# Performance work log

Hardware: AMD Instinct MI355X
Metric: run time of the kernel (lower is better)

## Reference

```python
import jax, jax.numpy as jnp
import numpy as np

N = 100000          # nodes
E = 800000          # edges
H = 32              # hidden_features
L = 4               # num_layers
HS = 32             # hidden_edge_scores
EPS_BN = 1e-5
EPS_AGG = 1e-6


def _bn(x, g, b):
    # training-mode batch norm over the node/edge (batch) axis
    mu = jnp.mean(x, axis=0)
    var = jnp.var(x, axis=0)
    return (x - mu) * jax.lax.rsqrt(var + EPS_BN) * g + b


def setup_inputs() -> dict:
    key = jax.random.key(0)
    ks = jax.random.split(key, 24)
    rn = lambda k, s, sc=0.1: jax.random.normal(k, s, dtype=jnp.float32) * sc
    return {
        "x": rn(ks[0], (N, 1), 1.0),
        "e": rn(ks[1], (E, 1), 1.0),
        "edge_index": jax.random.randint(ks[2], (2, E), 0, N),
        # input projections
        "pe_w": rn(ks[3], (1, H)), "pe_b": rn(ks[4], (H,)),
        "ed_w": rn(ks[5], (1, H)), "ed_b": rn(ks[6], (H,)),
        # per-layer GatedGCN weights, stacked over layers
        "A_w": rn(ks[7], (L, H, H)), "A_b": rn(ks[8], (L, H)),
        "B_w": rn(ks[9], (L, H, H)), "B_b": rn(ks[10], (L, H)),
        "C_w": rn(ks[11], (L, H, H)), "C_b": rn(ks[12], (L, H)),
        "U_w": rn(ks[13], (L, H, H)), "U_b": rn(ks[14], (L, H)),
        "V_w": rn(ks[15], (L, H, H)), "V_b": rn(ks[16], (L, H)),
        # batch-norm affine params
        "bn_h_g": jnp.ones((L, H), jnp.float32), "bn_h_b": jnp.zeros((L, H), jnp.float32),
        "bn_e_g": jnp.ones((L, H), jnp.float32), "bn_e_b": jnp.zeros((L, H), jnp.float32),
        # score predictor: concat(src_h, dst_h, e) -> HS -> 1
        "W1_w": rn(ks[17], (3 * H, HS)), "W1_b": rn(ks[18], (HS,)),
        "W2_w": rn(ks[19], (HS, 1)), "W2_b": rn(ks[20], (1,)),
    }


def reference(x, e, edge_index, pe_w, pe_b, ed_w, ed_b,
              A_w, A_b, B_w, B_b, C_w, C_b, U_w, U_b, V_w, V_b,
              bn_h_g, bn_h_b, bn_e_g, bn_e_b, W1_w, W1_b, W2_w, W2_b):
    src, dst = edge_index[0], edge_index[1]
    h = x @ pe_w + pe_b          # [N, H]
    e = e @ ed_w + ed_b          # [E, H]
    n = h.shape[0]
    for l in range(L):
        Ah = h @ A_w[l] + A_b[l]
        Bh = h @ B_w[l] + B_b[l]
        Ce = e @ C_w[l] + C_b[l]
        Uh = h @ U_w[l] + U_b[l]
        Vh = h @ V_w[l] + V_b[l]
        # edge update: gather node features to edges
        e_new = Ah[dst] + Bh[src] + Ce               # [E, H]
        sigma = jax.nn.sigmoid(e_new)                # edge gates
        # gated mean aggregation: scatter-add to dst nodes
        num = jax.ops.segment_sum(sigma * Vh[src], dst, num_segments=n)
        den = jax.ops.segment_sum(sigma, dst, num_segments=n)
        h_new = Uh + num / (den + EPS_AGG)           # [N, H]
        # BN -> ReLU -> residual
        h = h + jax.nn.relu(_bn(h_new, bn_h_g[l], bn_h_b[l]))
        e = e + jax.nn.relu(_bn(e_new, bn_e_g[l], bn_e_b[l]))
    # score predictor over edges
    z = jnp.concatenate([h[src], h[dst], e], axis=1)  # [E, 3H]
    scores = jax.nn.relu(z @ W1_w + W1_b) @ W2_w + W2_b  # [E, 1]
    return scores
```

## Files before the change

### kernel.cpp

```cpp
#include <hip/hip_runtime.h>
#include <hip/hip_bf16.h>
#include <hip/hip_fp16.h>

#define NLAYERS 4
#define GRID_STRIDE 2048

typedef _Float16 half8_t __attribute__((ext_vector_type(8)));
typedef float float4_t __attribute__((ext_vector_type(4)));
typedef float float8_t __attribute__((ext_vector_type(8)));

__global__ void zero_ints(int* __restrict__ p, int n)
{
    int i = blockIdx.x * 256 + threadIdx.x;
    if (i < n) p[i] = 0;
}

__global__ void hist_kernel(const int* __restrict__ dsts, int* __restrict__ counts, int E)
{
    int i = blockIdx.x * 256 + threadIdx.x;
    if (i < E) atomicAdd(&counts[dsts[i]], 1);
}

__global__ __launch_bounds__(256) void scan1(const int* __restrict__ counts,
                                             int* __restrict__ offsets,
                                             int* __restrict__ blocksums, int N)
{
    __shared__ int sdata[256];
    int t = threadIdx.x;
    int bbase = blockIdx.x * 1024;
    int v[4]; int s = 0;
#pragma unroll
    for (int q = 0; q < 4; q++) {
        int idx = bbase + t * 4 + q;
        v[q] = (idx < N) ? counts[idx] : 0;
        s += v[q];
    }
    sdata[t] = s;
    __syncthreads();
    for (int off = 1; off < 256; off <<= 1) {
        int x = (t >= off) ? sdata[t - off] : 0;
        __syncthreads();
        sdata[t] += x;
        __syncthreads();
    }
    int excl = sdata[t] - s;
    int run = excl;
#pragma unroll
    for (int q = 0; q < 4; q++) {
        int idx = bbase + t * 4 + q;
        if (idx < N) offsets[idx] = run;
        run += v[q];
    }
    if (t == 255) blocksums[blockIdx.x] = sdata[255];
}

__global__ void scan2(int* __restrict__ blocksums, int nb)
{
    if (threadIdx.x == 0 && blockIdx.x == 0) {
        int run = 0;
        for (int b = 0; b < nb; b++) { int t = blocksums[b]; blocksums[b] = run; run += t; }
    }
}

__global__ void scan3(int* __restrict__ offsets, const int* __restrict__ blocksums,
                      int* __restrict__ cursor, int N)
{
    int i = blockIdx.x * 256 + threadIdx.x;
    if (i < N) {
        int v = offsets[i] + blocksums[i >> 10];
        offsets[i] = v;
        cursor[i] = v;
    }
}

__global__ void scatter_perm(const int* __restrict__ dsts, int* __restrict__ cursor,
                             int* __restrict__ perm, int* __restrict__ pos, int E, int N)
{
    int g = blockIdx.x & 7;
    int lo = (int)((long long)N * g >> 3);
    int hi = (int)((long long)N * (g + 1) >> 3);
    int nbg = gridDim.x >> 3;
    int bg = blockIdx.x >> 3;
    for (int i = bg * 256 + threadIdx.x; i < E; i += nbg * 256) {
        int d = dsts[i];
        if (d >= lo && d < hi) {
            int slot = atomicAdd(&cursor[d], 1);
            perm[slot] = i;
            pos[i] = slot;
        }
    }
}

__global__ void gather_sd(const int* __restrict__ perm, const int* __restrict__ srcs,
                          const int* __restrict__ dsts, int* __restrict__ srcp,
                          int* __restrict__ dstp, int E)
{
    int i = blockIdx.x * 256 + threadIdx.x;
    if (i < E) {
        int e = perm[i];
        srcp[i] = srcs[e];
        dstp[i] = dsts[e];
    }
}

__global__ void init_proj4(const float* __restrict__ in, const float* __restrict__ w,
                           const float* __restrict__ b, float4* __restrict__ out, size_t n4)
{
    size_t i = (size_t)blockIdx.x * 256 + threadIdx.x;
    if (i < n4) {
        int j4 = (int)(i & 7) * 4;
        float xv = in[i >> 3];
        float4 wv = *(const float4*)(w + j4);
        float4 bv = *(const float4*)(b + j4);
        out[i] = make_float4(fmaf(xv, wv.x, bv.x), fmaf(xv, wv.y, bv.y),
                             fmaf(xv, wv.z, bv.z), fmaf(xv, wv.w, bv.w));
    }
}

__global__ void init_ep16(const float* __restrict__ e_in, const int* __restrict__ perm,
                          const float* __restrict__ w, const float* __restrict__ b,
                          __half2* __restrict__ out, size_t n4)
{
    size_t i = (size_t)blockIdx.x * 256 + threadIdx.x;
    if (i < n4) {
        int row = (int)(i >> 3);
        float xv = e_in[perm[row]];
        int j4 = (int)(i & 7) * 4;
        float4 wv = *(const float4*)(w + j4);
        float4 bv = *(const float4*)(b + j4);
        out[i * 2]     = __floats2half2_rn(fmaf(xv, wv.x, bv.x), fmaf(xv, wv.y, bv.y));
        out[i * 2 + 1] = __floats2half2_rn(fmaf(xv, wv.z, bv.z), fmaf(xv, wv.w, bv.w));
    }
}

template <int FUSE>
__global__ __launch_bounds__(256) void node_gemm(
    float* __restrict__ h, const float* __restrict__ hnew_in,
    const float* __restrict__ sc_h, const float* __restrict__ sh_h,
    const float* __restrict__ Aw, const float* __restrict__ Ab,
    const float* __restrict__ Bw, const float* __restrict__ Bb,
    const float* __restrict__ Uw, const float* __restrict__ Ub,
    const float* __restrict__ Vw, const float* __restrict__ Vb,
    __half* __restrict__ Ahh, __half* __restrict__ Bhh,
    float* __restrict__ Uhh, __half* __restrict__ Vhh, int N)
{
    int tid = threadIdx.x;
    int lane = tid & 63;
    int m = lane & 15, q = lane >> 4;
    half8_t bA0, bA1, bB0, bB1, bU0, bU1, bV0, bV1;
    float scq[8], shq[8];
#pragma unroll
    for (int i = 0; i < 8; i++) {
        int k = q * 8 + i;
        bA0[i] = (_Float16)Aw[k * 32 + m];  bA1[i] = (_Float16)Aw[k * 32 + m + 16];
        bB0[i] = (_Float16)Bw[k * 32 + m];  bB1[i] = (_Float16)Bw[k * 32 + m + 16];
        bU0[i] = (_Float16)Uw[k * 32 + m];  bU1[i] = (_Float16)Uw[k * 32 + m + 16];
        bV0[i] = (_Float16)Vw[k * 32 + m];  bV1[i] = (_Float16)Vw[k * 32 + m + 16];
        if (FUSE) { scq[i] = sc_h[k]; shq[i] = sh_h[k]; }
    }
    float ab0 = Ab[m], ab1 = Ab[m + 16];
    float bb0 = Bb[m], bb1 = Bb[m + 16];
    float ub0 = Ub[m], ub1 = Ub[m + 16];
    float vb0 = Vb[m], vb1 = Vb[m + 16];

    int ntile = (N + 15) >> 4;
    int wid = blockIdx.x * 4 + (tid >> 6);
    int nwave = gridDim.x * 4;
    for (int t = wid; t < ntile; t += nwave) {
        int base = t << 4;
        int arow = base + m;
        bool valid = arow < N;
        if (!valid) arow = N - 1;
        float8_t hv = *(const float8_t*)(h + (size_t)arow * 32 + q * 8);
        if (FUSE) {
            float8_t pv = *(const float8_t*)(hnew_in + (size_t)arow * 32 + q * 8);
#pragma unroll
            for (int i = 0; i < 8; i++)
                hv[i] += fmaxf(fmaf(pv[i], scq[i], shq[i]), 0.f);
            if (valid) *(float8_t*)(h + (size_t)arow * 32 + q * 8) = hv;
        }
        half8_t a;
#pragma unroll
        for (int i = 0; i < 8; i++) a[i] = (_Float16)hv[i];
        float4_t aA0 = __builtin_amdgcn_mfma_f32_16x16x32_f16(a, bA0, (float4_t){0,0,0,0}, 0, 0, 0);
        float4_t aA1 = __builtin_amdgcn_mfma_f32_16x16x32_f16(a, bA1, (float4_t){0,0,0,0}, 0, 0, 0);
        float4_t aB0 = __builtin_amdgcn_mfma_f32_16x16x32_f16(a, bB0, (float4_t){0,0,0,0}, 0, 0, 0);
        float4_t aB1 = __builtin_amdgcn_mfma_f32_16x16x32_f16(a, bB1, (float4_t){0,0,0,0}, 0, 0, 0);
        float4_t aU0 = __builtin_amdgcn_mfma_f32_16x16x32_f16(a, bU0, (float4_t){0,0,0,0}, 0, 0, 0);
        float4_t aU1 = __builtin_amdgcn_mfma_f32_16x16x32_f16(a, bU1, (float4_t){0,0,0,0}, 0, 0, 0);
        float4_t aV0 = __builtin_amdgcn_mfma_f32_16x16x32_f16(a, bV0, (float4_t){0,0,0,0}, 0, 0, 0);
        float4_t aV1 = __builtin_amdgcn_mfma_f32_16x16x32_f16(a, bV1, (float4_t){0,0,0,0}, 0, 0, 0);
#pragma unroll
        for (int reg = 0; reg < 4; reg++) {
            int node = base + q * 4 + reg;
            if (node < N) {
                size_t o = (size_t)node * 32;
                Ahh[o + m]      = __float2half_rn(aA0[reg] + ab0);
                Ahh[o + m + 16] = __float2half_rn(aA1[reg] + ab1);
                Bhh[o + m]      = __float2half_rn(aB0[reg] + bb0);
                Bhh[o + m + 16] = __float2half_rn(aB1[reg] + bb1);
                Vhh[o + m]      = __float2half_rn(aV0[reg] + vb0);
                Vhh[o + m + 16] = __float2half_rn(aV1[reg] + vb1);
                Uhh[o + m]      = aU0[reg] + ub0;
                Uhh[o + m + 16] = aU1[reg] + ub1;
            }
        }
    }
}

__global__ __launch_bounds__(256) void edge_en(
    const __half* __restrict__ ep,
    const int* __restrict__ srcp, const int* __restrict__ dstp,
    const __half* __restrict__ Ah, const __half* __restrict__ Bh,
    const float* __restrict__ Cw, const float* __restrict__ Cb,
    __half* __restrict__ enh, float* __restrict__ partial, int E)
{
    __shared__ float red[256];
    int tid = threadIdx.x;
    int lane = tid & 63;
    int m = lane & 15, q = lane >> 4;
    half8_t b0, b1;
#pragma unroll
    for (int i = 0; i < 8; i++) {
        int k = q * 8 + i;
        b0[i] = (_Float16)Cw[k * 32 + m];
        b1[i] = (_Float16)Cw[k * 32 + m + 16];
    }
    float cb0 = Cb[m], cb1 = Cb[m + 16];
    float es0 = 0.f, eq0 = 0.f, es1 = 0.f, eq1 = 0.f;

    int ntile = (E + 15) >> 4;
    int wid = blockIdx.x * 4 + (tid >> 6);
    int nwave = gridDim.x * 4;
    for (int t = wid; t < ntile; t += nwave) {
        int base = t << 4;
        int arow = base + m;
        if (arow >= E) arow = E - 1;
        half8_t a = *(const half8_t*)(ep + (size_t)arow * 32 + q * 8);
        float4_t acc0 = __builtin_amdgcn_mfma_f32_16x16x32_f16(a, b0, (float4_t){0.f,0.f,0.f,0.f}, 0, 0, 0);
        float4_t acc1 = __builtin_amdgcn_mfma_f32_16x16x32_f16(a, b1, (float4_t){0.f,0.f,0.f,0.f}, 0, 0, 0);
#pragma unroll
        for (int reg = 0; reg < 4; reg++) {
            int row = q * 4 + reg;
            int edge = base + row;
            if (edge < E) {
                int s = srcp[edge], d = dstp[edge];
                float ah0 = __half2float(Ah[(size_t)d * 32 + m]);
                float bh0 = __half2float(Bh[(size_t)s * 32 + m]);
                float ah1 = __half2float(Ah[(size_t)d * 32 + m + 16]);
                float bh1 = __half2float(Bh[(size_t)s * 32 + m + 16]);
                float en0 = acc0[reg] + cb0 + ah0 + bh0;
                float en1 = acc1[reg] + cb1 + ah1 + bh1;
                enh[(size_t)edge * 32 + m]      = __float2half_rn(en0);
                enh[(size_t)edge * 32 + m + 16] = __float2half_rn(en1);
                es0 += en0; eq0 += en0 * en0;
                es1 += en1; eq1 += en1 * en1;
            }
        }
    }
    float* p = partial + (size_t)blockIdx.x * 64;
    __syncthreads();
    red[tid] = es0;
    __syncthreads();
    if (tid < 16) {
        float s = 0.f;
#pragma unroll
        for (int w = 0; w < 4; w++)
#pragma unroll
            for (int k = 0; k < 4; k++) s += red[w * 64 + k * 16 + tid];
        p[tid] = s;
    }
    __syncthreads();
    red[tid] = es1;
    __syncthreads();
    if (tid < 16) {
        float s = 0.f;
#pragma unroll
        for (int w = 0; w < 4; w++)
#pragma unroll
            for (int k = 0; k < 4; k++) s += red[w * 64 + k * 16 + tid];
        p[16 + tid] = s;
    }
    __syncthreads();
    red[tid] = eq0;
    __syncthreads();
    if (tid < 16) {
        float s = 0.f;
#pragma unroll
        for (int w = 0; w < 4; w++)
#pragma unroll
            for (int k = 0; k < 4; k++) s += red[w * 64 + k * 16 + tid];
        p[32 + tid] = s;
    }
    __syncthreads();
    red[tid] = eq1;
    __syncthreads();
    if (tid < 16) {
        float s = 0.f;
#pragma unroll
        for (int w = 0; w < 4; w++)
#pragma unroll
            for (int k = 0; k < 4; k++) s += red[w * 64 + k * 16 + tid];
        p[48 + tid] = s;
    }
}

__global__ __launch_bounds__(256) void node_agg(
    const __half* __restrict__ enh, const int* __restrict__ srcp,
    const int* __restrict__ offsets, const int* __restrict__ counts,
    const __half* __restrict__ Vh, float* __restrict__ hnew,
    __half* __restrict__ ep, const float* __restrict__ sc_e, const float* __restrict__ sh_e,
    float* __restrict__ partial, int N)
{
    __shared__ float red[512];
    int tid = threadIdx.x, u = tid & 15, grp = tid >> 4;
    int c0 = 2 * u;
    float sc0 = sc_e[c0], sh0 = sh_e[c0];
    float sc1 = sc_e[c0 + 1], sh1 = sh_e[c0 + 1];
    float hs0 = 0.f, hq0 = 0.f, hs1 = 0.f, hq1 = 0.f;
    for (int nb0 = blockIdx.x * 16; nb0 < N; nb0 += gridDim.x * 16) {
        int node = nb0 + grp;
        if (node >= N) break;
        int start = offsets[node], len = counts[node];
        float num0 = 0.f, den0 = 0.f, num1 = 0.f, den1 = 0.f;
        int qq = 0;
        for (; qq + 2 <= len; qq += 2) {
            int p0 = start + qq, p1 = p0 + 1;
            int s0 = srcp[p0], s1 = srcp[p1];
            float2 en0 = __half22float2(*(const __half2*)(enh + (size_t)p0 * 32 + c0));
            float2 en1 = __half22float2(*(const __half2*)(enh + (size_t)p1 * 32 + c0));
            float2 vh0 = __half22float2(*(const __half2*)(Vh + (size_t)s0 * 32 + c0));
            float2 vh1 = __half22float2(*(const __half2*)(Vh + (size_t)s1 * 32 + c0));
            float2 e0 = __half22float2(*(const __half2*)(ep + (size_t)p0 * 32 + c0));
            float2 e1 = __half22float2(*(const __half2*)(ep + (size_t)p1 * 32 + c0));
            float sg00 = 1.f / (1.f + __expf(-en0.x)), sg01 = 1.f / (1.f + __expf(-en0.y));
            float sg10 = 1.f / (1.f + __expf(-en1.x)), sg11 = 1.f / (1.f + __expf(-en1.y));
            num0 = fmaf(sg00, vh0.x, num0); num1 = fmaf(sg01, vh0.y, num1);
            num0 = fmaf(sg10, vh1.x, num0); num1 = fmaf(sg11, vh1.y, num1);
            den0 += sg00 + sg10; den1 += sg01 + sg11;
            *(__half2*)(ep + (size_t)p0 * 32 + c0) = __floats2half2_rn(
                e0.x + fmaxf(fmaf(en0.x, sc0, sh0), 0.f),
                e0.y + fmaxf(fmaf(en0.y, sc1, sh1), 0.f));
            *(__half2*)(ep + (size_t)p1 * 32 + c0) = __floats2half2_rn(
                e1.x + fmaxf(fmaf(en1.x, sc0, sh0), 0.f),
                e1.y + fmaxf(fmaf(en1.y, sc1, sh1), 0.f));
        }
        if (qq < len) {
            int p0 = start + qq;
            int s0 = srcp[p0];
            float2 en0 = __half22float2(*(const __half2*)(enh + (size_t)p0 * 32 + c0));
            float2 vh0 = __half22float2(*(const __half2*)(Vh + (size_t)s0 * 32 + c0));
            float2 e0 = __half22float2(*(const __half2*)(ep + (size_t)p0 * 32 + c0));
            float sg00 = 1.f / (1.f + __expf(-en0.x)), sg01 = 1.f / (1.f + __expf(-en0.y));
            num0 = fmaf(sg00, vh0.x, num0); num1 = fmaf(sg01, vh0.y, num1);
            den0 += sg00; den1 += sg01;
            *(__half2*)(ep + (size_t)p0 * 32 + c0) = __floats2half2_rn(
                e0.x + fmaxf(fmaf(en0.x, sc0, sh0), 0.f),
                e0.y + fmaxf(fmaf(en0.y, sc1, sh1), 0.f));
        }
        size_t ho = (size_t)node * 32 + c0;
        float hv0 = hnew[ho]     + num0 / (den0 + 1e-6f);
        float hv1 = hnew[ho + 1] + num1 / (den1 + 1e-6f);
        *(float2*)(hnew + ho) = make_float2(hv0, hv1);
        hs0 += hv0; hq0 += hv0 * hv0;
        hs1 += hv1; hq1 += hv1 * hv1;
    }
    __syncthreads();
    red[tid] = hs0; red[256 + tid] = hs1;
    __syncthreads();
    float* p = partial + (size_t)blockIdx.x * 64;
    if (tid < 32) {
        int uu = tid >> 1, par = tid & 1;
        const float* r = red + par * 256;
        float s = 0.f;
#pragma unroll
        for (int g = 0; g < 16; g++) s += r[g * 16 + uu];
        p[tid] = s;
    }
    __syncthreads();
    red[tid] = hq0; red[256 + tid] = hq1;
    __syncthreads();
    if (tid < 32) {
        int uu = tid >> 1, par = tid & 1;
        const float* r = red + par * 256;
        float s = 0.f;
#pragma unroll
        for (int g = 0; g < 16; g++) s += r[g * 16 + uu];
        p[32 + tid] = s;
    }
}

__global__ __launch_bounds__(256) void stats_side(
    const float* __restrict__ partial, int nrows, double cnt,
    const float* __restrict__ g, const float* __restrict__ b,
    float* __restrict__ sc_out, float* __restrict__ sh_out)
{
    int j = blockIdx.x;
    __shared__ double rs[256], rq[256];
    double s = 0.0, q = 0.0;
    for (int r = threadIdx.x; r < nrows; r += 256) {
        s += (double)partial[(size_t)r * 64 + j];
        q += (double)partial[(size_t)r * 64 + 32 + j];
    }
    rs[threadIdx.x] = s; rq[threadIdx.x] = q;
    __syncthreads();
    for (int off = 128; off; off >>= 1) {
        if (threadIdx.x < off) { rs[threadIdx.x] += rs[threadIdx.x + off]; rq[threadIdx.x] += rq[threadIdx.x + off]; }
        __syncthreads();
    }
    if (threadIdx.x == 0) {
        double mean = rs[0] / cnt;
        double var = rq[0] / cnt - mean * mean;
        float scale = g[j] * (float)(1.0 / sqrt(var + 1e-5));
        sc_out[j] = scale;
        sh_out[j] = b[j] - (float)mean * scale;
    }
}

__global__ void apply4_h16(const float4* __restrict__ pre, const float* __restrict__ scale,
                           const float* __restrict__ shift, const float4* __restrict__ hold,
                           __half2* __restrict__ h16, size_t n4)
{
    size_t i = (size_t)blockIdx.x * 256 + threadIdx.x;
    if (i < n4) {
        int j4 = (int)(i & 7) * 4;
        float4 sc = *(const float4*)(scale + j4);
        float4 sh = *(const float4*)(shift + j4);
        float4 p = pre[i], a = hold[i];
        a.x += fmaxf(fmaf(p.x, sc.x, sh.x), 0.f);
        a.y += fmaxf(fmaf(p.y, sc.y, sh.y), 0.f);
        a.z += fmaxf(fmaf(p.z, sc.z, sh.z), 0.f);
        a.w += fmaxf(fmaf(p.w, sc.w, sh.w), 0.f);
        h16[i * 2]     = __floats2half2_rn(a.x, a.y);
        h16[i * 2 + 1] = __floats2half2_rn(a.z, a.w);
    }
}

__global__ __launch_bounds__(256) void predictor(
    const __half* __restrict__ h16, const __half* __restrict__ e16,
    const int* __restrict__ srcs, const int* __restrict__ dsts, const int* __restrict__ pos,
    const float* __restrict__ W1, const float* __restrict__ b1,
    const float* __restrict__ W2, const float* __restrict__ b2v,
    float* __restrict__ out, int E)
{
    int tid = threadIdx.x;
    int lane = tid & 63;
    int m = lane & 15, q = lane >> 4;
    half8_t bf00, bf01, bf10, bf11, bf20, bf21;
#pragma unroll
    for (int i = 0; i < 8; i++) {
        int k = q * 8 + i;
        bf00[i] = (_Float16)W1[k * 32 + m];
        bf01[i] = (_Float16)W1[k * 32 + m + 16];
        bf10[i] = (_Float16)W1[(32 + k) * 32 + m];
        bf11[i] = (_Float16)W1[(32 + k) * 32 + m + 16];
        bf20[i] = (_Float16)W1[(64 + k) * 32 + m];
        bf21[i] = (_Float16)W1[(64 + k) * 32 + m + 16];
    }
    float b10 = b1[m], b11 = b1[m + 16];
    float w20 = W2[m], w21 = W2[m + 16];
    float b2 = b2v[0];

    int ntile = (E + 15) >> 4;
    int wid = blockIdx.x * 4 + (tid >> 6);
    int nwave = gridDim.x * 4;
    for (int t = wid; t < ntile; t += nwave) {
        int base = t << 4;
        int arow = base + m;
        if (arow >= E) arow = E - 1;
        int s = srcs[arow], d = dsts[arow];
        int erow = pos[arow];
        half8_t a0 = *(const half8_t*)(h16 + (size_t)s * 32 + q * 8);
        half8_t a1 = *(const half8_t*)(h16 + (size_t)d * 32 + q * 8);
        half8_t a2 = *(const half8_t*)(e16 + (size_t)erow * 32 + q * 8);
        float4_t acc0 = {0.f, 0.f, 0.f, 0.f}, acc1 = {0.f, 0.f, 0.f, 0.f};
        acc0 = __builtin_amdgcn_mfma_f32_16x16x32_f16(a0, bf00, acc0, 0, 0, 0);
        acc1 = __builtin_amdgcn_mfma_f32_16x16x32_f16(a0, bf01, acc1, 0, 0, 0);
        acc0 = __builtin_amdgcn_mfma_f32_16x16x32_f16(a1, bf10, acc0, 0, 0, 0);
        acc1 = __builtin_amdgcn_mfma_f32_16x16x32_f16(a1, bf11, acc1, 0, 0, 0);
        acc0 = __builtin_amdgcn_mfma_f32_16x16x32_f16(a2, bf20, acc0, 0, 0, 0);
        acc1 = __builtin_amdgcn_mfma_f32_16x16x32_f16(a2, bf21, acc1, 0, 0, 0);
#pragma unroll
        for (int reg = 0; reg < 4; reg++) {
            float tp = fmaxf(acc0[reg] + b10, 0.f) * w20
                     + fmaxf(acc1[reg] + b11, 0.f) * w21;
            tp += __shfl_xor(tp, 1);
            tp += __shfl_xor(tp, 2);
            tp += __shfl_xor(tp, 4);
            tp += __shfl_xor(tp, 8);
            int edge = base + q * 4 + reg;
            if (m == 0 && edge < E) out[edge] = tp + b2;
        }
    }
}

extern "C" void kernel_launch(void* const* d_in, const int* in_sizes, int n_in,
                              void* d_out, int out_size, void* d_ws, size_t ws_size,
                              hipStream_t stream)
{
    const int N = in_sizes[0];
    const int E = in_sizes[1];

    const float* x    = (const float*)d_in[0];
    const float* e_in = (const float*)d_in[1];
    const int*   eidx = (const int*)d_in[2];
    const float* pe_w = (const float*)d_in[3];
    const float* pe_b = (const float*)d_in[4];
    const float* ed_w = (const float*)d_in[5];
    const float* ed_b = (const float*)d_in[6];
    const float* Aw = (const float*)d_in[7];
    const float* Ab = (const float*)d_in[8];
    const float* Bw = (const float*)d_in[9];
    const float* Bb = (const float*)d_in[10];
    const float* Cw = (const float*)d_in[11];
    const float* Cb = (const float*)d_in[12];
    const float* Uw = (const float*)d_in[13];
    const float* Ub = (const float*)d_in[14];
    const float* Vw = (const float*)d_in[15];
    const float* Vb = (const float*)d_in[16];
    const float* bn_h_g = (const float*)d_in[17];
    const float* bn_h_b = (const float*)d_in[18];
    const float* bn_e_g = (const float*)d_in[19];
    const float* bn_e_b = (const float*)d_in[20];
    const float* W1w = (const float*)d_in[21];
    const float* W1b = (const float*)d_in[22];
    const float* W2w = (const float*)d_in[23];
    const float* W2b = (const float*)d_in[24];

    const int* srcs = eidx;
    const int* dsts = eidx + E;

    size_t nh = (size_t)N * 32;
    size_t eh = (size_t)E * 32;

    float* ws = (float*)d_ws;
    float* stats     = ws;
    float* partial_h = stats + 128;
    float* partial_e = partial_h + GRID_STRIDE * 64;
    float* h    = partial_e + GRID_STRIDE * 64;
    float* hnew = h + nh;
    __half* Ah  = (__half*)(hnew + nh);
    __half* Bh  = Ah + nh;
    __half* Vh  = Bh + nh;
    __half* ep  = Vh + nh;
    __half* enh = ep + eh;
    int* counts    = (int*)(enh + eh);
    int* offsets   = counts + N;
    int* cursor    = offsets + N;
    int* blocksums = cursor + N;
    int* perm      = blocksums + 128;
    int* srcp      = perm + E;
    int* dstp      = srcp + E;
    int* pos       = dstp + E;

    size_t nh4 = nh / 4, eh4 = eh / 4;
    int gh4 = (int)((nh4 + 255) / 256);
    int ge4 = (int)((eh4 + 255) / 256);
    int gN = (N + 255) / 256;
    int gE = (E + 255) / 256;
    int nb = (N + 1023) / 1024;
    int ntileN = (N + 15) / 16;
    int gGemm = (ntileN + 3) / 4;
    if (gGemm > GRID_STRIDE) gGemm = GRID_STRIDE;

    zero_ints<<<gN, 256, 0, stream>>>(counts, N);
    hist_kernel<<<gE, 256, 0, stream>>>(dsts, counts, E);
    scan1<<<nb, 256, 0, stream>>>(counts, offsets, blocksums, N);
    scan2<<<1, 64, 0, stream>>>(blocksums, nb);
    scan3<<<gN, 256, 0, stream>>>(offsets, blocksums, cursor, N);
    scatter_perm<<<GRID_STRIDE, 256, 0, stream>>>(dsts, cursor, perm, pos, E, N);
    gather_sd<<<gE, 256, 0, stream>>>(perm, srcs, dsts, srcp, dstp, E);

    init_proj4<<<gh4, 256, 0, stream>>>(x, pe_w, pe_b, (float4*)h, nh4);
    init_ep16<<<ge4, 256, 0, stream>>>(e_in, perm, ed_w, ed_b, (__half2*)ep, eh4);

    for (int l = 0; l < NLAYERS; l++) {
        if (l == 0)
            node_gemm<0><<<gGemm, 256, 0, stream>>>(h, hnew, stats + 0, stats + 32,
                Aw + l * 1024, Ab + l * 32, Bw + l * 1024, Bb + l * 32,
                Uw + l * 1024, Ub + l * 32, Vw + l * 1024, Vb + l * 32,
                Ah, Bh, hnew, Vh, N);
        else
            node_gemm<1><<<gGemm, 256, 0, stream>>>(h, hnew, stats + 0, stats + 32,
                Aw + l * 1024, Ab + l * 32, Bw + l * 1024, Bb + l * 32,
                Uw + l * 1024, Ub + l * 32, Vw + l * 1024, Vb + l * 32,
                Ah, Bh, hnew, Vh, N);
        edge_en<<<GRID_STRIDE, 256, 0, stream>>>(ep, srcp, dstp, Ah, Bh,
            Cw + l * 1024, Cb + l * 32, enh, partial_e, E);
        stats_side<<<32, 256, 0, stream>>>(partial_e, GRID_STRIDE, (double)E,
            bn_e_g + l * 32, bn_e_b + l * 32, stats + 64, stats + 96);
        node_agg<<<GRID_STRIDE, 256, 0, stream>>>(enh, srcp, offsets, counts,
            Vh, hnew, ep, stats + 64, stats + 96, partial_h, N);
        stats_side<<<32, 256, 0, stream>>>(partial_h, GRID_STRIDE, (double)N,
            bn_h_g + l * 32, bn_h_b + l * 32, stats + 0, stats + 32);
    }

    apply4_h16<<<gh4, 256, 0, stream>>>((const float4*)hnew, stats + 0, stats + 32,
                                        (const float4*)h, (__half2*)Ah, nh4);

    predictor<<<GRID_STRIDE, 256, 0, stream>>>((const __half*)Ah, (const __half*)ep,
                                               srcs, dsts, pos, W1w, W1b, W2w, W2b,
                                               (float*)d_out, E);
}
```

Baseline: 714.1 us.

## Interleave hidden-feature columns for packed stores and iterate predictor in sorted edge order

Stores node and edge feature columns in an interleaved order (column 2m holds original m, column 2m+1 holds original m+16), so each MFMA lane can write half2/float2 pairs instead of scalar halves. The weight rows, BN gamma/beta and stats indices are permuted to match. node_agg now processes 4 columns per thread with 8-byte loads, and the predictor walks edges in dst-sorted order, scattering outputs through perm, which removes the pos array. The cost is scattered 4-byte output writes in the predictor, and correctness depends on every consumer applying the column permutation consistently.

```diff
diff --git a/kernel.cpp b/kernel.cpp
--- a/kernel.cpp
+++ b/kernel.cpp
@@ -8,6 +8,23 @@
 typedef _Float16 half8_t __attribute__((ext_vector_type(8)));
 typedef float float4_t __attribute__((ext_vector_type(4)));
 typedef float float8_t __attribute__((ext_vector_type(8)));
+
+__device__ __forceinline__ int permcol(int pos) { return (pos >> 1) | ((pos & 1) << 4); }
+
+__device__ __forceinline__ void unp4(uint2 r, float* f)
+{
+    float2 a = __half22float2(*(__half2*)&r.x);
+    float2 b = __half22float2(*(__half2*)&r.y);
+    f[0] = a.x; f[1] = a.y; f[2] = b.x; f[3] = b.y;
+}
+
+__device__ __forceinline__ uint2 pk4(float f0, float f1, float f2, float f3)
+{
+    __half2 a = __floats2half2_rn(f0, f1), b = __floats2half2_rn(f2, f3);
+    uint2 r;
+    r.x = *(unsigned*)&a; r.y = *(unsigned*)&b;
+    return r;
+}
 
 __global__ void zero_ints(int* __restrict__ p, int n)
 {
@@ -74,7 +91,7 @@
 }
 
 __global__ void scatter_perm(const int* __restrict__ dsts, int* __restrict__ cursor,
-                             int* __restrict__ perm, int* __restrict__ pos, int E, int N)
+                             int* __restrict__ perm, int E, int N)
 {
     int g = blockIdx.x & 7;
     int lo = (int)((long long)N * g >> 3);
@@ -86,7 +103,6 @@
         if (d >= lo && d < hi) {
             int slot = atomicAdd(&cursor[d], 1);
             perm[slot] = i;
-            pos[i] = slot;
         }
     }
 }
@@ -110,10 +126,9 @@
     if (i < n4) {
         int j4 = (int)(i & 7) * 4;
         float xv = in[i >> 3];
-        float4 wv = *(const float4*)(w + j4);
-        float4 bv = *(const float4*)(b + j4);
-        out[i] = make_float4(fmaf(xv, wv.x, bv.x), fmaf(xv, wv.y, bv.y),
-                             fmaf(xv, wv.z, bv.z), fmaf(xv, wv.w, bv.w));
+        int c0 = permcol(j4), c1 = permcol(j4 + 1), c2 = permcol(j4 + 2), c3 = permcol(j4 + 3);
+        out[i] = make_float4(fmaf(xv, w[c0], b[c0]), fmaf(xv, w[c1], b[c1]),
+                             fmaf(xv, w[c2], b[c2]), fmaf(xv, w[c3], b[c3]));
     }
 }
 
@@ -126,10 +141,9 @@
         int row = (int)(i >> 3);
         float xv = e_in[perm[row]];
         int j4 = (int)(i & 7) * 4;
-        float4 wv = *(const float4*)(w + j4);
-        float4 bv = *(const float4*)(b + j4);
-        out[i * 2]     = __floats2half2_rn(fmaf(xv, wv.x, bv.x), fmaf(xv, wv.y, bv.y));
-        out[i * 2 + 1] = __floats2half2_rn(fmaf(xv, wv.z, bv.z), fmaf(xv, wv.w, bv.w));
+        int c0 = permcol(j4), c1 = permcol(j4 + 1), c2 = permcol(j4 + 2), c3 = permcol(j4 + 3);
+        out[i * 2]     = __floats2half2_rn(fmaf(xv, w[c0], b[c0]), fmaf(xv, w[c1], b[c1]));
+        out[i * 2 + 1] = __floats2half2_rn(fmaf(xv, w[c2], b[c2]), fmaf(xv, w[c3], b[c3]));
     }
 }
 
@@ -152,10 +166,11 @@
 #pragma unroll
     for (int i = 0; i < 8; i++) {
         int k = q * 8 + i;
-        bA0[i] = (_Float16)Aw[k * 32 + m];  bA1[i] = (_Float16)Aw[k * 32 + m + 16];
-        bB0[i] = (_Float16)Bw[k * 32 + m];  bB1[i] = (_Float16)Bw[k * 32 + m + 16];
-        bU0[i] = (_Float16)Uw[k * 32 + m];  bU1[i] = (_Float16)Uw[k * 32 + m + 16];
-        bV0[i] = (_Float16)Vw[k * 32 + m];  bV1[i] = (_Float16)Vw[k * 32 + m + 16];
+        int kr = permcol(k);
+        bA0[i] = (_Float16)Aw[kr * 32 + m];  bA1[i] = (_Float16)Aw[kr * 32 + m + 16];
+        bB0[i] = (_Float16)Bw[kr * 32 + m];  bB1[i] = (_Float16)Bw[kr * 32 + m + 16];
+        bU0[i] = (_Float16)Uw[kr * 32 + m];  bU1[i] = (_Float16)Uw[kr * 32 + m + 16];
+        bV0[i] = (_Float16)Vw[kr * 32 + m];  bV1[i] = (_Float16)Vw[kr * 32 + m + 16];
         if (FUSE) { scq[i] = sc_h[k]; shq[i] = sh_h[k]; }
     }
     float ab0 = Ab[m], ab1 = Ab[m + 16];
@@ -195,14 +210,10 @@
             int node = base + q * 4 + reg;
             if (node < N) {
                 size_t o = (size_t)node * 32;
-                Ahh[o + m]      = __float2half_rn(aA0[reg] + ab0);
-                Ahh[o + m + 16] = __float2half_rn(aA1[reg] + ab1);
-                Bhh[o + m]      = __float2half_rn(aB0[reg] + bb0);
-                Bhh[o + m + 16] = __float2half_rn(aB1[reg] + bb1);
-                Vhh[o + m]      = __float2half_rn(aV0[reg] + vb0);
-                Vhh[o + m + 16] = __float2half_rn(aV1[reg] + vb1);
-                Uhh[o + m]      = aU0[reg] + ub0;
-                Uhh[o + m + 16] = aU1[reg] + ub1;
+                *(__half2*)(Ahh + o + 2 * m) = __floats2half2_rn(aA0[reg] + ab0, aA1[reg] + ab1);
+                *(__half2*)(Bhh + o + 2 * m) = __floats2half2_rn(aB0[reg] + bb0, aB1[reg] + bb1);
+                *(__half2*)(Vhh + o + 2 * m) = __floats2half2_rn(aV0[reg] + vb0, aV1[reg] + vb1);
+                *(float2*)(Uhh + o + 2 * m)  = make_float2(aU0[reg] + ub0, aU1[reg] + ub1);
             }
         }
     }
@@ -223,8 +234,9 @@
 #pragma unroll
     for (int i = 0; i < 8; i++) {
         int k = q * 8 + i;
-        b0[i] = (_Float16)Cw[k * 32 + m];
-        b1[i] = (_Float16)Cw[k * 32 + m + 16];
+        int kr = permcol(k);
+        b0[i] = (_Float16)Cw[kr * 32 + m];
+        b1[i] = (_Float16)Cw[kr * 32 + m + 16];
     }
     float cb0 = Cb[m], cb1 = Cb[m + 16];
     float es0 = 0.f, eq0 = 0.f, es1 = 0.f, eq1 = 0.f;
@@ -245,14 +257,11 @@
             int edge = base + row;
             if (edge < E) {
                 int s = srcp[edge], d = dstp[edge];
-                float ah0 = __half2float(Ah[(size_t)d * 32 + m]);
-                float bh0 = __half2float(Bh[(size_t)s * 32 + m]);
-                float ah1 = __half2float(Ah[(size_t)d * 32 + m + 16]);
-                float bh1 = __half2float(Bh[(size_t)s * 32 + m + 16]);
-                float en0 = acc0[reg] + cb0 + ah0 + bh0;
-                float en1 = acc1[reg] + cb1 + ah1 + bh1;
-                enh[(size_t)edge * 32 + m]      = __float2half_rn(en0);
-                enh[(size_t)edge * 32 + m + 16] = __float2half_rn(en1);
+                float2 ah = __half22float2(*(const __half2*)(Ah + (size_t)d * 32 + 2 * m));
+                float2 bh = __half22float2(*(const __half2*)(Bh + (size_t)s * 32 + 2 * m));
+                float en0 = acc0[reg] + cb0 + ah.x + bh.x;
+                float en1 = acc1[reg] + cb1 + ah.y + bh.y;
+                *(__half2*)(enh + (size_t)edge * 32 + 2 * m) = __floats2half2_rn(en0, en1);
                 es0 += en0; eq0 += en0 * en0;
                 es1 += en1; eq1 += en1 * en1;
             }
@@ -268,7 +277,7 @@
         for (int w = 0; w < 4; w++)
 #pragma unroll
             for (int k = 0; k < 4; k++) s += red[w * 64 + k * 16 + tid];
-        p[tid] = s;
+        p[2 * tid] = s;
     }
     __syncthreads();
     red[tid] = es1;
@@ -279,7 +288,7 @@
         for (int w = 0; w < 4; w++)
 #pragma unroll
             for (int k = 0; k < 4; k++) s += red[w * 64 + k * 16 + tid];
-        p[16 + tid] = s;
+        p[2 * tid + 1] = s;
     }
     __syncthreads();
     red[tid] = eq0;
@@ -290,7 +299,7 @@
         for (int w = 0; w < 4; w++)
 #pragma unroll
             for (int k = 0; k < 4; k++) s += red[w * 64 + k * 16 + tid];
-        p[32 + tid] = s;
+        p[32 + 2 * tid] = s;
     }
     __syncthreads();
     red[tid] = eq1;
@@ -301,7 +310,7 @@
         for (int w = 0; w < 4; w++)
 #pragma unroll
             for (int k = 0; k < 4; k++) s += red[w * 64 + k * 16 + tid];
-        p[48 + tid] = s;
+        p[32 + 2 * tid + 1] = s;
     }
 }
 
@@ -313,80 +322,94 @@
     float* __restrict__ partial, int N)
 {
     __shared__ float red[512];
-    int tid = threadIdx.x, u = tid & 15, grp = tid >> 4;
-    int c0 = 2 * u;
-    float sc0 = sc_e[c0], sh0 = sh_e[c0];
-    float sc1 = sc_e[c0 + 1], sh1 = sh_e[c0 + 1];
-    float hs0 = 0.f, hq0 = 0.f, hs1 = 0.f, hq1 = 0.f;
-    for (int nb0 = blockIdx.x * 16; nb0 < N; nb0 += gridDim.x * 16) {
+    int tid = threadIdx.x, u = tid & 7, grp = tid >> 3;
+    int c0 = 4 * u;
+    float sc[4], sh[4];
+#pragma unroll
+    for (int k = 0; k < 4; k++) { sc[k] = sc_e[c0 + k]; sh[k] = sh_e[c0 + k]; }
+    float hs[4] = {0.f, 0.f, 0.f, 0.f}, hq[4] = {0.f, 0.f, 0.f, 0.f};
+
+    for (int nb0 = blockIdx.x * 32; nb0 < N; nb0 += gridDim.x * 32) {
         int node = nb0 + grp;
         if (node >= N) break;
         int start = offsets[node], len = counts[node];
-        float num0 = 0.f, den0 = 0.f, num1 = 0.f, den1 = 0.f;
+        float num[4] = {0.f, 0.f, 0.f, 0.f}, den[4] = {0.f, 0.f, 0.f, 0.f};
         int qq = 0;
         for (; qq + 2 <= len; qq += 2) {
             int p0 = start + qq, p1 = p0 + 1;
             int s0 = srcp[p0], s1 = srcp[p1];
-            float2 en0 = __half22float2(*(const __half2*)(enh + (size_t)p0 * 32 + c0));
-            float2 en1 = __half22float2(*(const __half2*)(enh + (size_t)p1 * 32 + c0));
-            float2 vh0 = __half22float2(*(const __half2*)(Vh + (size_t)s0 * 32 + c0));
-            float2 vh1 = __half22float2(*(const __half2*)(Vh + (size_t)s1 * 32 + c0));
-            float2 e0 = __half22float2(*(const __half2*)(ep + (size_t)p0 * 32 + c0));
-            float2 e1 = __half22float2(*(const __half2*)(ep + (size_t)p1 * 32 + c0));
-            float sg00 = 1.f / (1.f + __expf(-en0.x)), sg01 = 1.f / (1.f + __expf(-en0.y));
-            float sg10 = 1.f / (1.f + __expf(-en1.x)), sg11 = 1.f / (1.f + __expf(-en1.y));
-            num0 = fmaf(sg00, vh0.x, num0); num1 = fmaf(sg01, vh0.y, num1);
-            num0 = fmaf(sg10, vh1.x, num0); num1 = fmaf(sg11, vh1.y, num1);
-            den0 += sg00 + sg10; den1 += sg01 + sg11;
-            *(__half2*)(ep + (size_t)p0 * 32 + c0) = __floats2half2_rn(
-                e0.x + fmaxf(fmaf(en0.x, sc0, sh0), 0.f),
-                e0.y + fmaxf(fmaf(en0.y, sc1, sh1), 0.f));
-            *(__half2*)(ep + (size_t)p1 * 32 + c0) = __floats2half2_rn(
-                e1.x + fmaxf(fmaf(en1.x, sc0, sh0), 0.f),
-                e1.y + fmaxf(fmaf(en1.y, sc1, sh1), 0.f));
+            uint2 enr0 = *(const uint2*)(enh + (size_t)p0 * 32 + c0);
+            uint2 enr1 = *(const uint2*)(enh + (size_t)p1 * 32 + c0);
+            uint2 vhr0 = *(const uint2*)(Vh + (size_t)s0 * 32 + c0);
+            uint2 vhr1 = *(const uint2*)(Vh + (size_t)s1 * 32 + c0);
+            uint2 epr0 = *(const uint2*)(ep + (size_t)p0 * 32 + c0);
+            uint2 epr1 = *(const uint2*)(ep + (size_t)p1 * 32 + c0);
+            float en0[4], en1[4], vh0[4], vh1[4], ev0[4], ev1[4];
+            unp4(enr0, en0); unp4(enr1, en1);
+            unp4(vhr0, vh0); unp4(vhr1, vh1);
+            unp4(epr0, ev0); unp4(epr1, ev1);
+            float o0[4], o1[4];
+#pragma unroll
+            for (int k = 0; k < 4; k++) {
+                float sg0 = 1.f / (1.f + __expf(-en0[k]));
+                float sg1 = 1.f / (1.f + __expf(-en1[k]));
+                num[k] = fmaf(sg0, vh0[k], num[k]);
+                num[k] = fmaf(sg1, vh1[k], num[k]);
+                den[k] += sg0 + sg1;
+                o0[k] = ev0[k] + fmaxf(fmaf(en0[k], sc[k], sh[k]), 0.f);
+                o1[k] = ev1[k] + fmaxf(fmaf(en1[k], sc[k], sh[k]), 0.f);
+            }
+            *(uint2*)(ep + (size_t)p0 * 32 + c0) = pk4(o0[0], o0[1], o0[2], o0[3]);
+            *(uint2*)(ep + (size_t)p1 * 32 + c0) = pk4(o1[0], o1[1], o1[2], o1[3]);
         }
         if (qq < len) {
             int p0 = start + qq;
             int s0 = srcp[p0];
-            float2 en0 = __half22float2(*(const __half2*)(enh + (size_t)p0 * 32 + c0));
-            float2 vh0 = __half22float2(*(const __half2*)(Vh + (size_t)s0 * 32 + c0));
-            float2 e0 = __half22float2(*(const __half2*)(ep + (size_t)p0 * 32 + c0));
-            float sg00 = 1.f / (1.f + __expf(-en0.x)), sg01 = 1.f / (1.f + __expf(-en0.y));
-            num0 = fmaf(sg00, vh0.x, num0); num1 = fmaf(sg01, vh0.y, num1);
-            den0 += sg00; den1 += sg01;
-            *(__half2*)(ep + (size_t)p0 * 32 + c0) = __floats2half2_rn(
-                e0.x + fmaxf(fmaf(en0.x, sc0, sh0), 0.f),
-                e0.y + fmaxf(fmaf(en0.y, sc1, sh1), 0.f));
+            uint2 enr0 = *(const uint2*)(enh + (size_t)p0 * 32 + c0);
+            uint2 vhr0 = *(const uint2*)(Vh + (size_t)s0 * 32 + c0);
+            uint2 epr0 = *(const uint2*)(ep + (size_t)p0 * 32 + c0);
+            float en0[4], vh0[4], ev0[4];
+            unp4(enr0, en0); unp4(vhr0, vh0); unp4(epr0, ev0);
+            float o0[4];
+#pragma unroll
+            for (int k = 0; k < 4; k++) {
+                float sg0 = 1.f / (1.f + __expf(-en0[k]));
+                num[k] = fmaf(sg0, vh0[k], num[k]);
+                den[k] += sg0;
+                o0[k] = ev0[k] + fmaxf(fmaf(en0[k], sc[k], sh[k]), 0.f);
+            }
+            *(uint2*)(ep + (size_t)p0 * 32 + c0) = pk4(o0[0], o0[1], o0[2], o0[3]);
         }
         size_t ho = (size_t)node * 32 + c0;
-        float hv0 = hnew[ho]     + num0 / (den0 + 1e-6f);
-        float hv1 = hnew[ho + 1] + num1 / (den1 + 1e-6f);
-        *(float2*)(hnew + ho) = make_float2(hv0, hv1);
-        hs0 += hv0; hq0 += hv0 * hv0;
-        hs1 += hv1; hq1 += hv1 * hv1;
-    }
-    __syncthreads();
-    red[tid] = hs0; red[256 + tid] = hs1;
-    __syncthreads();
+        float4 uh = *(const float4*)(hnew + ho);
+        float hv[4];
+        hv[0] = uh.x + num[0] / (den[0] + 1e-6f);
+        hv[1] = uh.y + num[1] / (den[1] + 1e-6f);
+        hv[2] = uh.z + num[2] / (den[2] + 1e-6f);
+        hv[3] = uh.w + num[3] / (den[3] + 1e-6f);
+        *(float4*)(hnew + ho) = make_float4(hv[0], hv[1], hv[2], hv[3]);
+#pragma unroll
+        for (int k = 0; k < 4; k++) { hs[k] += hv[k]; hq[k] += hv[k] * hv[k]; }
+    }
+
     float* p = partial + (size_t)blockIdx.x * 64;
-    if (tid < 32) {
-        int uu = tid >> 1, par = tid & 1;
-        const float* r = red + par * 256;
-        float s = 0.f;
-#pragma unroll
-        for (int g = 0; g < 16; g++) s += r[g * 16 + uu];
-        p[tid] = s;
-    }
-    __syncthreads();
-    red[tid] = hq0; red[256 + tid] = hq1;
-    __syncthreads();
-    if (tid < 32) {
-        int uu = tid >> 1, par = tid & 1;
-        const float* r = red + par * 256;
-        float s = 0.f;
-#pragma unroll
-        for (int g = 0; g < 16; g++) s += r[g * 16 + uu];
-        p[32 + tid] = s;
+#pragma unroll
+    for (int k = 0; k < 4; k++) {
+        __syncthreads();
+        red[tid] = hs[k]; red[256 + tid] = hq[k];
+        __syncthreads();
+        if (tid < 8) {
+            float s = 0.f;
+#pragma unroll
+            for (int g = 0; g < 32; g++) s += red[g * 8 + tid];
+            p[4 * tid + k] = s;
+        } else if (tid < 16) {
+            int uu = tid - 8;
+            float s = 0.f;
+#pragma unroll
+            for (int g = 0; g < 32; g++) s += red[256 + g * 8 + uu];
+            p[32 + 4 * uu + k] = s;
+        }
     }
 }
 
@@ -396,6 +419,7 @@
     float* __restrict__ sc_out, float* __restrict__ sh_out)
 {
     int j = blockIdx.x;
+    int col = (j >> 1) | ((j & 1) << 4);
     __shared__ double rs[256], rq[256];
     double s = 0.0, q = 0.0;
     for (int r = threadIdx.x; r < nrows; r += 256) {
@@ -411,9 +435,9 @@
     if (threadIdx.x == 0) {
         double mean = rs[0] / cnt;
         double var = rq[0] / cnt - mean * mean;
-        float scale = g[j] * (float)(1.0 / sqrt(var + 1e-5));
+        float scale = g[col] * (float)(1.0 / sqrt(var + 1e-5));
         sc_out[j] = scale;
-        sh_out[j] = b[j] - (float)mean * scale;
+        sh_out[j] = b[col] - (float)mean * scale;
     }
 }
 
@@ -438,7 +462,7 @@
 
 __global__ __launch_bounds__(256) void predictor(
     const __half* __restrict__ h16, const __half* __restrict__ e16,
-    const int* __restrict__ srcs, const int* __restrict__ dsts, const int* __restrict__ pos,
+    const int* __restrict__ srcp, const int* __restrict__ dstp, const int* __restrict__ perm,
     const float* __restrict__ W1, const float* __restrict__ b1,
     const float* __restrict__ W2, const float* __restrict__ b2v,
     float* __restrict__ out, int E)
@@ -450,12 +474,13 @@
 #pragma unroll
     for (int i = 0; i < 8; i++) {
         int k = q * 8 + i;
-        bf00[i] = (_Float16)W1[k * 32 + m];
-        bf01[i] = (_Float16)W1[k * 32 + m + 16];
-        bf10[i] = (_Float16)W1[(32 + k) * 32 + m];
-        bf11[i] = (_Float16)W1[(32 + k) * 32 + m + 16];
-        bf20[i] = (_Float16)W1[(64 + k) * 32 + m];
-        bf21[i] = (_Float16)W1[(64 + k) * 32 + m + 16];
+        int kr = permcol(k);
+        bf00[i] = (_Float16)W1[kr * 32 + m];
+        bf01[i] = (_Float16)W1[kr * 32 + m + 16];
+        bf10[i] = (_Float16)W1[(32 + kr) * 32 + m];
+        bf11[i] = (_Float16)W1[(32 + kr) * 32 + m + 16];
+        bf20[i] = (_Float16)W1[(64 + kr) * 32 + m];
+        bf21[i] = (_Float16)W1[(64 + kr) * 32 + m + 16];
     }
     float b10 = b1[m], b11 = b1[m + 16];
     float w20 = W2[m], w21 = W2[m + 16];
@@ -468,11 +493,10 @@
         int base = t << 4;
         int arow = base + m;
         if (arow >= E) arow = E - 1;
-        int s = srcs[arow], d = dsts[arow];
-        int erow = pos[arow];
+        int s = srcp[arow], d = dstp[arow];
         half8_t a0 = *(const half8_t*)(h16 + (size_t)s * 32 + q * 8);
         half8_t a1 = *(const half8_t*)(h16 + (size_t)d * 32 + q * 8);
-        half8_t a2 = *(const half8_t*)(e16 + (size_t)erow * 32 + q * 8);
+        half8_t a2 = *(const half8_t*)(e16 + (size_t)arow * 32 + q * 8);
         float4_t acc0 = {0.f, 0.f, 0.f, 0.f}, acc1 = {0.f, 0.f, 0.f, 0.f};
         acc0 = __builtin_amdgcn_mfma_f32_16x16x32_f16(a0, bf00, acc0, 0, 0, 0);
         acc1 = __builtin_amdgcn_mfma_f32_16x16x32_f16(a0, bf01, acc1, 0, 0, 0);
@@ -488,8 +512,11 @@
             tp += __shfl_xor(tp, 2);
             tp += __shfl_xor(tp, 4);
             tp += __shfl_xor(tp, 8);
-            int edge = base + q * 4 + reg;
-            if (m == 0 && edge < E) out[edge] = tp + b2;
+            int idx = base + q * 4 + reg;
+            if (m == 0 && idx < E) {
+                int oe = perm[idx];
+                out[oe] = tp + b2;
+            }
         }
     }
 }
@@ -551,7 +578,6 @@
     int* perm      = blocksums + 128;
     int* srcp      = perm + E;
     int* dstp      = srcp + E;
-    int* pos       = dstp + E;
 
     size_t nh4 = nh / 4, eh4 = eh / 4;
     int gh4 = (int)((nh4 + 255) / 256);
@@ -568,7 +594,7 @@
     scan1<<<nb, 256, 0, stream>>>(counts, offsets, blocksums, N);
     scan2<<<1, 64, 0, stream>>>(blocksums, nb);
     scan3<<<gN, 256, 0, stream>>>(offsets, blocksums, cursor, N);
-    scatter_perm<<<GRID_STRIDE, 256, 0, stream>>>(dsts, cursor, perm, pos, E, N);
+    scatter_perm<<<GRID_STRIDE, 256, 0, stream>>>(dsts, cursor, perm, E, N);
     gather_sd<<<gE, 256, 0, stream>>>(perm, srcs, dsts, srcp, dstp, E);
 
     init_proj4<<<gh4, 256, 0, stream>>>(x, pe_w, pe_b, (float4*)h, nh4);
@@ -599,6 +625,6 @@
                                         (const float4*)h, (__half2*)Ah, nh4);
 
     predictor<<<GRID_STRIDE, 256, 0, stream>>>((const __half*)Ah, (const __half*)ep,
-                                               srcs, dsts, pos, W1w, W1b, W2w, W2b,
+                                               srcp, dstp, perm, W1w, W1b, W2w, W2b,
                                                (float*)d_out, E);
 }
```

Measured after the change: 723.3 us. About the same (+1.3%).
